# Optimization experiments

Hardware: AMD Instinct MI355X
Metric: run time of the kernel (lower is better)

## Reference

```python
import jax, jax.numpy as jnp
import numpy as np

B, NPIX, M, N_CP, N_CA = 8, 256, 8192, 24576, 24576
EPS = 1e-16


def setup_inputs() -> dict:
    key = jax.random.key(0)
    k1, k2, k3, k4, k5, k6 = jax.random.split(key, 6)
    images = jax.random.normal(k1, (B, NPIX, NPIX), dtype=jnp.float32)
    # k-space trajectory in radians/pixel, range [-pi, pi) as torchkbnufft expects
    ktraj = (jax.random.uniform(k2, (2, M), dtype=jnp.float32) * 2.0 - 1.0) * np.float32(np.pi)
    pulsefac = jax.random.normal(k3, (2, M), dtype=jnp.float32)
    cphase_sign = jnp.sign(jax.random.normal(k4, (3, N_CP), dtype=jnp.float32))
    cphase_ind = jax.random.randint(k5, (3, N_CP), 0, M, dtype=jnp.int32)
    camp_ind = jax.random.randint(k6, (4, N_CA), 0, M, dtype=jnp.int32)
    return {"images": images, "ktraj": ktraj, "pulsefac": pulsefac,
            "cphase_sign": cphase_sign, "cphase_ind": cphase_ind, "camp_ind": camp_ind}


def reference(images, ktraj, pulsefac, cphase_sign, cphase_ind, camp_ind):
    npix = images.shape[-1]
    # centered image coordinates (Fessler NUFFT convention, n_shift = npix//2)
    coords = (jnp.arange(npix) - npix // 2).astype(jnp.float32)
    kv, ku = ktraj[0], ktraj[1]  # (M,) each
    # separable exact NDFT: exp(-i(kv*y + ku*x)) = Ev[m,y] * Eu[m,x]
    Ev = jnp.exp(-1j * kv[:, None] * coords[None, :]).astype(jnp.complex64)  # (M, npix)
    Eu = jnp.exp(-1j * ku[:, None] * coords[None, :]).astype(jnp.complex64)  # (M, npix)
    img_c = images.astype(jnp.complex64)
    tmp = jnp.einsum('byx,my->bmx', img_c, Ev)        # (B, M, npix)
    kdata = jnp.einsum('bmx,mx->bm', tmp, Eu)          # (B, M) complex visibilities
    # pulse-function correction (complex multiply)
    pf = pulsefac[0] + 1j * pulsefac[1]                # (M,)
    vis_c = kdata * pf                                 # (B, M)
    vis = jnp.stack([vis_c.real, vis_c.imag], axis=1)  # (B, 2, M)
    visamp = jnp.sqrt(vis_c.real ** 2 + vis_c.imag ** 2 + EPS)  # (B, M)
    # closure phases: gather triangle visibilities, signed phase sum, degrees
    v_tri = vis_c[:, cphase_ind]                       # (B, 3, N_cp)
    ang = jnp.arctan2(v_tri.imag, v_tri.real)          # (B, 3, N_cp)
    cphase = jnp.einsum('kn,bkn->bn', cphase_sign, ang) * np.float32(180.0 / np.pi)
    # log closure amplitudes: gather quadrangle visibilities
    v_quad = vis_c[:, camp_ind]                        # (B, 4, N_ca)
    amp = jnp.sqrt(v_quad.real ** 2 + v_quad.imag ** 2 + EPS)
    logcamp = (jnp.log(amp[:, 0]) + jnp.log(amp[:, 1])
               - jnp.log(amp[:, 2]) - jnp.log(amp[:, 3]))  # (B, N_ca)
    return vis, visamp, cphase, logcamp
```

## Files before the change

### kernel.cpp

```cpp
#include <hip/hip_runtime.h>
#include <cmath>

#define BB   8
#define NPIX 256
#define MM   8192
#define NCP  24576
#define NCA  24576
#define EPSF 1e-16f

#define KC   32
#define TMB  128
#define NT   512

#define VIS_OFF    0
#define VISAMP_OFF (BB * 2 * MM)
#define CPH_OFF    (VISAMP_OFF + BB * MM)
#define LCA_OFF    (CPH_OFF + BB * NCP)

typedef __bf16 bf16x8 __attribute__((ext_vector_type(8)));
typedef float  f32x4  __attribute__((ext_vector_type(4)));

#define WIDX(row, k8) (((row) >> 4) * 512 + (k8) * 128 + ((row) & 15) * 8)

__device__ __forceinline__ float red2pi(float k, float n)
{
    const double t = (double)k * (double)n * 0.15915494309189535;
    const double f = t - rint(t);
    return (float)(f * 6.283185307179586);
}

__global__ __launch_bounds__(NT, 2)
void nufft_vis_mfma(const float* __restrict__ images,
                    const float* __restrict__ ktraj,
                    const float* __restrict__ pulsefac,
                    float* __restrict__ out)
{
    __shared__ __align__(16) __bf16 sBh[NPIX * KC];
    __shared__ __align__(16) __bf16 sBl[NPIX * KC];

    const int tid  = threadIdx.x;
    const int m0   = blockIdx.x * TMB;
    const int b    = blockIdx.y;
    const int lane = tid & 63;
    const int w    = tid >> 6;
    const int ln15 = lane & 15;
    const int q    = lane >> 4;

    const float kvm = ktraj[m0 + w * 16 + ln15];
    float r1s, r1c, r32s, r32c, as_, ac_;
    sincosf(kvm, &r1s, &r1c);
    sincosf(red2pi(kvm, 32.0f), &r32s, &r32c);
    sincosf(red2pi(kvm, (float)(q * 8 - 128)), &as_, &ac_);
    float anr = ac_, ani = -as_;

    const int bx    = tid & 255;
    const int bhalf = tid >> 8;
    const float* imgb = images + b * NPIX * NPIX + bx;

    f32x4 acc[2][16];
    #pragma unroll
    for (int rt = 0; rt < 2; ++rt)
        #pragma unroll
        for (int ct = 0; ct < 16; ++ct)
            acc[rt][ct] = (f32x4){0.f, 0.f, 0.f, 0.f};

    for (int y0 = 0; y0 < NPIX; y0 += KC) {
        bf16x8 fRh, fRl, fIh, fIl;
        {
            float er = anr, ei = ani;
            #pragma unroll
            for (int j = 0; j < 8; ++j) {
                __bf16 h = (__bf16)er;
                fRh[j] = h; fRl[j] = (__bf16)(er - (float)h);
                h = (__bf16)ei;
                fIh[j] = h; fIl[j] = (__bf16)(ei - (float)h);
                const float nr = er * r1c + ei * r1s;
                const float ni = ei * r1c - er * r1s;
                er = nr; ei = ni;
            }
            const float nr = anr * r32c + ani * r32s;
            const float ni = ani * r32c - anr * r32s;
            anr = nr; ani = ni;
        }
        #pragma unroll
        for (int oo = 0; oo < 2; ++oo) {
            const int oct = bhalf * 2 + oo;
            bf16x8 bh, bl;
            #pragma unroll
            for (int j = 0; j < 8; ++j) {
                const float v = imgb[(y0 + oct * 8 + j) * NPIX];
                const __bf16 h = (__bf16)v;
                bh[j] = h; bl[j] = (__bf16)(v - (float)h);
            }
            const int bo = WIDX(bx, oct);
            *(bf16x8*)&sBh[bo] = bh;
            *(bf16x8*)&sBl[bo] = bl;
        }
        __syncthreads();

        #pragma unroll
        for (int ct = 0; ct < 16; ++ct) {
            const int bro = WIDX(ct * 16 + ln15, q);
            const bf16x8 bh = *(const bf16x8*)&sBh[bro];
            const bf16x8 bl = *(const bf16x8*)&sBl[bro];
            acc[0][ct] = __builtin_amdgcn_mfma_f32_16x16x32_bf16(fRh, bh, acc[0][ct], 0, 0, 0);
            acc[0][ct] = __builtin_amdgcn_mfma_f32_16x16x32_bf16(fRh, bl, acc[0][ct], 0, 0, 0);
            acc[0][ct] = __builtin_amdgcn_mfma_f32_16x16x32_bf16(fRl, bh, acc[0][ct], 0, 0, 0);
            acc[1][ct] = __builtin_amdgcn_mfma_f32_16x16x32_bf16(fIh, bh, acc[1][ct], 0, 0, 0);
            acc[1][ct] = __builtin_amdgcn_mfma_f32_16x16x32_bf16(fIh, bl, acc[1][ct], 0, 0, 0);
            acc[1][ct] = __builtin_amdgcn_mfma_f32_16x16x32_bf16(fIl, bh, acc[1][ct], 0, 0, 0);
        }
        __syncthreads();
    }

    #pragma unroll
    for (int r = 0; r < 4; ++r) {
        const int m = m0 + w * 16 + q * 4 + r;
        const float ku = ktraj[MM + m];
        float s0, c0, s16, c16;
        sincosf(red2pi(ku, (float)(ln15 - 128)), &s0, &c0);
        sincosf(red2pi(ku, 16.0f), &s16, &c16);
        float er = c0, ei = -s0;
        float sr = 0.f, si = 0.f;
        #pragma unroll
        for (int ct = 0; ct < 16; ++ct) {
            const float tr = acc[0][ct][r];
            const float ti = acc[1][ct][r];
            sr = fmaf(tr, er, fmaf(-ti, ei, sr));
            si = fmaf(tr, ei, fmaf(ti, er, si));
            const float nr = er * c16 + ei * s16;
            const float ni = ei * c16 - er * s16;
            er = nr; ei = ni;
        }
        #pragma unroll
        for (int off = 8; off >= 1; off >>= 1) {
            sr += __shfl_xor(sr, off);
            si += __shfl_xor(si, off);
        }
        if (ln15 == 0) {
            const float pr = pulsefac[m];
            const float pi = pulsefac[MM + m];
            const float vr = sr * pr - si * pi;
            const float vi = sr * pi + si * pr;
            out[b * 2 * MM + m]      = vr;
            out[b * 2 * MM + MM + m] = vi;
            out[VISAMP_OFF + b * MM + m] = sqrtf(vr * vr + vi * vi + EPSF);
        }
    }
}

__device__ __forceinline__ float fast_atan2f(float y, float x)
{
    const float ax = fabsf(x), ay = fabsf(y);
    const float mx = fmaxf(ax, ay), mn = fminf(ax, ay);
    const float a  = mn / fmaxf(mx, 1e-37f);
    const float s  = a * a;
    float r = 0.0208351f;
    r = fmaf(r, s, -0.0851330f);
    r = fmaf(r, s,  0.1801410f);
    r = fmaf(r, s, -0.3302995f);
    r = fmaf(r, s,  0.9998660f);
    r *= a;
    r = (ay > ax) ? (1.57079632679f - r) : r;
    r = (x < 0.0f) ? (3.14159265359f - r) : r;
    return (y < 0.0f) ? -r : r;
}

__global__ __launch_bounds__(256)
void gather_fused(const float* __restrict__ vis,
                  const float* __restrict__ sign,
                  const int* __restrict__ cind,
                  const int* __restrict__ caind,
                  float* __restrict__ out)
{
    __shared__ float sv[2 * MM];

    const int i = blockIdx.x * 256 + threadIdx.x;
    const int b = i / NCP;
    const int n = i - b * NCP;

    {
        const float4* g4 = (const float4*)(vis + b * 2 * MM);
        float4* s4 = (float4*)sv;
        #pragma unroll
        for (int j = 0; j < (2 * MM / 4) / 256; ++j)
            s4[j * 256 + threadIdx.x] = g4[j * 256 + threadIdx.x];
    }
    __syncthreads();

    float cp = 0.f;
    #pragma unroll
    for (int k = 0; k < 3; ++k) {
        const int m = cind[k * NCP + n];
        cp += sign[k * NCP + n] * fast_atan2f(sv[MM + m], sv[m]);
    }
    out[CPH_OFF + i] = cp * 57.29577951308232f;

    float p[4];
    #pragma unroll
    for (int k = 0; k < 4; ++k) {
        const int m = caind[k * NCA + n];
        const float vr = sv[m];
        const float vi = sv[MM + m];
        p[k] = vr * vr + vi * vi + EPSF;
    }
    out[LCA_OFF + i] = 0.5f * __logf((p[0] * p[1]) / (p[2] * p[3]));
}

extern "C" void kernel_launch(void* const* d_in, const int* in_sizes, int n_in,
                              void* d_out, int out_size, void* d_ws, size_t ws_size,
                              hipStream_t stream)
{
    const float* images   = (const float*)d_in[0];
    const float* ktraj    = (const float*)d_in[1];
    const float* pulsefac = (const float*)d_in[2];
    const float* csign    = (const float*)d_in[3];
    const int*   cind     = (const int*)d_in[4];
    const int*   caind    = (const int*)d_in[5];
    float* out = (float*)d_out;

    dim3 grid(MM / TMB, BB);
    nufft_vis_mfma<<<grid, NT, 0, stream>>>(images, ktraj, pulsefac, out);
    gather_fused<<<BB * NCP / 256, 256, 0, stream>>>(out, csign, cind, caind, out);
}
```

Before: 116.9 us.

## Software-pipeline image loads and twiddle generation behind MFMA, halve block tile

Halves the block size to 256 threads and 64 k-space rows, so each thread now stages a full image column slice. The next K-chunk's global image loads are issued before the current MFMA loop, and the bf16 split conversion and next A-fragment twiddle generation run after it, all with a fully unrolled chunk loop. The aim is to hide global load latency and VALU work behind the matrix ops. In exchange, every block now reloads the whole image, doubling image traffic and staging work per output, and register pressure rises under launch bounds of one block per CU.

```diff
diff --git a/kernel.cpp b/kernel.cpp
--- a/kernel.cpp
+++ b/kernel.cpp
@@ -9,8 +9,8 @@
 #define EPSF 1e-16f
 
 #define KC   32
-#define TMB  128
-#define NT   512
+#define TMB  64
+#define NT   256
 
 #define VIS_OFF    0
 #define VISAMP_OFF (BB * 2 * MM)
@@ -29,7 +29,7 @@
     return (float)(f * 6.283185307179586);
 }
 
-__global__ __launch_bounds__(NT, 2)
+__global__ __launch_bounds__(NT, 1)
 void nufft_vis_mfma(const float* __restrict__ images,
                     const float* __restrict__ ktraj,
                     const float* __restrict__ pulsefac,
@@ -53,9 +53,53 @@
     sincosf(red2pi(kvm, (float)(q * 8 - 128)), &as_, &ac_);
     float anr = ac_, ani = -as_;
 
-    const int bx    = tid & 255;
-    const int bhalf = tid >> 8;
-    const float* imgb = images + b * NPIX * NPIX + bx;
+    const float* imgb = images + b * NPIX * NPIX + tid;
+
+    bf16x8 fRh[2], fRl[2], fIh[2], fIl[2];
+    float  lv[4][8];
+    bf16x8 sbh[4], sbl[4];
+
+    auto genA = [&](int slot) {
+        float er = anr, ei = ani;
+        #pragma unroll
+        for (int j = 0; j < 8; ++j) {
+            __bf16 h = (__bf16)er;
+            fRh[slot][j] = h; fRl[slot][j] = (__bf16)(er - (float)h);
+            h = (__bf16)ei;
+            fIh[slot][j] = h; fIl[slot][j] = (__bf16)(ei - (float)h);
+            const float nr = er * r1c + ei * r1s;
+            const float ni = ei * r1c - er * r1s;
+            er = nr; ei = ni;
+        }
+        const float nr = anr * r32c + ani * r32s;
+        const float ni = ani * r32c - anr * r32s;
+        anr = nr; ani = ni;
+    };
+    auto loadB = [&](int y0) {
+        #pragma unroll
+        for (int oct = 0; oct < 4; ++oct)
+            #pragma unroll
+            for (int j = 0; j < 8; ++j)
+                lv[oct][j] = imgb[(y0 + oct * 8 + j) * NPIX];
+    };
+    auto convB = [&]() {
+        #pragma unroll
+        for (int oct = 0; oct < 4; ++oct)
+            #pragma unroll
+            for (int j = 0; j < 8; ++j) {
+                const float v = lv[oct][j];
+                const __bf16 h = (__bf16)v;
+                sbh[oct][j] = h; sbl[oct][j] = (__bf16)(v - (float)h);
+            }
+    };
+    auto writeB = [&]() {
+        #pragma unroll
+        for (int oct = 0; oct < 4; ++oct) {
+            const int bo = WIDX(tid, oct);
+            *(bf16x8*)&sBh[bo] = sbh[oct];
+            *(bf16x8*)&sBl[bo] = sbl[oct];
+        }
+    };
 
     f32x4 acc[2][16];
     #pragma unroll
@@ -64,53 +108,36 @@
         for (int ct = 0; ct < 16; ++ct)
             acc[rt][ct] = (f32x4){0.f, 0.f, 0.f, 0.f};
 
-    for (int y0 = 0; y0 < NPIX; y0 += KC) {
-        bf16x8 fRh, fRl, fIh, fIl;
-        {
-            float er = anr, ei = ani;
-            #pragma unroll
-            for (int j = 0; j < 8; ++j) {
-                __bf16 h = (__bf16)er;
-                fRh[j] = h; fRl[j] = (__bf16)(er - (float)h);
-                h = (__bf16)ei;
-                fIh[j] = h; fIl[j] = (__bf16)(ei - (float)h);
-                const float nr = er * r1c + ei * r1s;
-                const float ni = ei * r1c - er * r1s;
-                er = nr; ei = ni;
-            }
-            const float nr = anr * r32c + ani * r32s;
-            const float ni = ani * r32c - anr * r32s;
-            anr = nr; ani = ni;
-        }
-        #pragma unroll
-        for (int oo = 0; oo < 2; ++oo) {
-            const int oct = bhalf * 2 + oo;
-            bf16x8 bh, bl;
-            #pragma unroll
-            for (int j = 0; j < 8; ++j) {
-                const float v = imgb[(y0 + oct * 8 + j) * NPIX];
-                const __bf16 h = (__bf16)v;
-                bh[j] = h; bl[j] = (__bf16)(v - (float)h);
-            }
-            const int bo = WIDX(bx, oct);
-            *(bf16x8*)&sBh[bo] = bh;
-            *(bf16x8*)&sBl[bo] = bl;
-        }
+    genA(0);
+    loadB(0);
+    convB();
+    writeB();
+
+    #pragma unroll
+    for (int c = 0; c < 8; ++c) {
+        const int cur = c & 1;
         __syncthreads();
+        if (c < 7) loadB((c + 1) * KC);
 
         #pragma unroll
         for (int ct = 0; ct < 16; ++ct) {
             const int bro = WIDX(ct * 16 + ln15, q);
             const bf16x8 bh = *(const bf16x8*)&sBh[bro];
             const bf16x8 bl = *(const bf16x8*)&sBl[bro];
-            acc[0][ct] = __builtin_amdgcn_mfma_f32_16x16x32_bf16(fRh, bh, acc[0][ct], 0, 0, 0);
-            acc[0][ct] = __builtin_amdgcn_mfma_f32_16x16x32_bf16(fRh, bl, acc[0][ct], 0, 0, 0);
-            acc[0][ct] = __builtin_amdgcn_mfma_f32_16x16x32_bf16(fRl, bh, acc[0][ct], 0, 0, 0);
-            acc[1][ct] = __builtin_amdgcn_mfma_f32_16x16x32_bf16(fIh, bh, acc[1][ct], 0, 0, 0);
-            acc[1][ct] = __builtin_amdgcn_mfma_f32_16x16x32_bf16(fIh, bl, acc[1][ct], 0, 0, 0);
-            acc[1][ct] = __builtin_amdgcn_mfma_f32_16x16x32_bf16(fIl, bh, acc[1][ct], 0, 0, 0);
+            acc[0][ct] = __builtin_amdgcn_mfma_f32_16x16x32_bf16(fRh[cur], bh, acc[0][ct], 0, 0, 0);
+            acc[0][ct] = __builtin_amdgcn_mfma_f32_16x16x32_bf16(fRh[cur], bl, acc[0][ct], 0, 0, 0);
+            acc[0][ct] = __builtin_amdgcn_mfma_f32_16x16x32_bf16(fRl[cur], bh, acc[0][ct], 0, 0, 0);
+            acc[1][ct] = __builtin_amdgcn_mfma_f32_16x16x32_bf16(fIh[cur], bh, acc[1][ct], 0, 0, 0);
+            acc[1][ct] = __builtin_amdgcn_mfma_f32_16x16x32_bf16(fIh[cur], bl, acc[1][ct], 0, 0, 0);
+            acc[1][ct] = __builtin_amdgcn_mfma_f32_16x16x32_bf16(fIl[cur], bh, acc[1][ct], 0, 0, 0);
+        }
+
+        if (c < 7) {
+            genA(cur ^ 1);
+            convB();
         }
         __syncthreads();
+        if (c < 7) writeB();
     }
 
     #pragma unroll
```

Result: slower. 142.3 us (+21.7%).

## Switch NUFFT GEMM to 32x32x16 MFMA with swapped operands and 2D wave tiling

Applied to the files above, without the earlier changes.

Replaces the 16x16x32 MFMA tiling with 32x32x16 MFMA. The image tile becomes the A operand and the per-lane trajectory phase vector becomes B. Waves are split 4x2 over m and x, and a cross-wave reduction through shared memory is added at the end. The Eu phase-rotation epilogue is rewritten to match the new accumulator layout. The aim is higher MFMA throughput per instruction and less LDS traffic per flop, at the cost of an extra reduction step and a more complex phase recurrence.

```diff
diff --git a/kernel.cpp b/kernel.cpp
--- a/kernel.cpp
+++ b/kernel.cpp
@@ -19,8 +19,9 @@
 
 typedef __bf16 bf16x8 __attribute__((ext_vector_type(8)));
 typedef float  f32x4  __attribute__((ext_vector_type(4)));
-
-#define WIDX(row, k8) (((row) >> 4) * 512 + (k8) * 128 + ((row) & 15) * 8)
+typedef float  f32x16 __attribute__((ext_vector_type(16)));
+
+#define WIDX32(x, o) (((x) >> 5) * 1024 + (o) * 256 + ((x) & 31) * 8)
 
 __device__ __forceinline__ float red2pi(float k, float n)
 {
@@ -43,45 +44,55 @@
     const int b    = blockIdx.y;
     const int lane = tid & 63;
     const int w    = tid >> 6;
-    const int ln15 = lane & 15;
-    const int q    = lane >> 4;
-
-    const float kvm = ktraj[m0 + w * 16 + ln15];
-    float r1s, r1c, r32s, r32c, as_, ac_;
+    const int wm   = w >> 1;
+    const int wx   = w & 1;
+    const int l31  = lane & 31;
+    const int hi   = lane >> 5;
+
+    const int mlane = m0 + wm * 32 + l31;
+    const float kvm = ktraj[mlane];
+    float r1s, r1c, r16s, r16c, as_, ac_;
     sincosf(kvm, &r1s, &r1c);
-    sincosf(red2pi(kvm, 32.0f), &r32s, &r32c);
-    sincosf(red2pi(kvm, (float)(q * 8 - 128)), &as_, &ac_);
+    sincosf(red2pi(kvm, 16.0f), &r16s, &r16c);
+    sincosf(red2pi(kvm, (float)(hi * 8 - 128)), &as_, &ac_);
     float anr = ac_, ani = -as_;
 
     const int bx    = tid & 255;
     const int bhalf = tid >> 8;
     const float* imgb = images + b * NPIX * NPIX + bx;
 
-    f32x4 acc[2][16];
+    auto genB = [&](bf16x8& Rh, bf16x8& Rl, bf16x8& Ih, bf16x8& Il) {
+        float er = anr, ei = ani;
+        #pragma unroll
+        for (int j = 0; j < 8; ++j) {
+            __bf16 h = (__bf16)er;
+            Rh[j] = h; Rl[j] = (__bf16)(er - (float)h);
+            h = (__bf16)ei;
+            Ih[j] = h; Il[j] = (__bf16)(ei - (float)h);
+            const float nr = er * r1c + ei * r1s;
+            const float ni = ei * r1c - er * r1s;
+            er = nr; ei = ni;
+        }
+        const float nr = anr * r16c + ani * r16s;
+        const float ni = ani * r16c - anr * r16s;
+        anr = nr; ani = ni;
+    };
+
+    f32x16 acc[2][4];
     #pragma unroll
-    for (int rt = 0; rt < 2; ++rt)
-        #pragma unroll
-        for (int ct = 0; ct < 16; ++ct)
-            acc[rt][ct] = (f32x4){0.f, 0.f, 0.f, 0.f};
-
-    for (int y0 = 0; y0 < NPIX; y0 += KC) {
-        bf16x8 fRh, fRl, fIh, fIl;
-        {
-            float er = anr, ei = ani;
+    for (int p = 0; p < 2; ++p)
+        #pragma unroll
+        for (int xt = 0; xt < 4; ++xt)
             #pragma unroll
-            for (int j = 0; j < 8; ++j) {
-                __bf16 h = (__bf16)er;
-                fRh[j] = h; fRl[j] = (__bf16)(er - (float)h);
-                h = (__bf16)ei;
-                fIh[j] = h; fIl[j] = (__bf16)(ei - (float)h);
-                const float nr = er * r1c + ei * r1s;
-                const float ni = ei * r1c - er * r1s;
-                er = nr; ei = ni;
-            }
-            const float nr = anr * r32c + ani * r32s;
-            const float ni = ani * r32c - anr * r32s;
-            anr = nr; ani = ni;
-        }
+            for (int rg = 0; rg < 16; ++rg)
+                acc[p][xt][rg] = 0.f;
+
+    for (int c = 0; c < NPIX / KC; ++c) {
+        const int y0 = c * KC;
+
+        bf16x8 eRh, eRl, eIh, eIl;
+        genB(eRh, eRl, eIh, eIl);
+
         #pragma unroll
         for (int oo = 0; oo < 2; ++oo) {
             const int oct = bhalf * 2 + oo;
@@ -92,60 +103,88 @@
                 const __bf16 h = (__bf16)v;
                 bh[j] = h; bl[j] = (__bf16)(v - (float)h);
             }
-            const int bo = WIDX(bx, oct);
+            const int bo = WIDX32(bx, oct);
             *(bf16x8*)&sBh[bo] = bh;
             *(bf16x8*)&sBl[bo] = bl;
         }
         __syncthreads();
 
         #pragma unroll
-        for (int ct = 0; ct < 16; ++ct) {
-            const int bro = WIDX(ct * 16 + ln15, q);
-            const bf16x8 bh = *(const bf16x8*)&sBh[bro];
-            const bf16x8 bl = *(const bf16x8*)&sBl[bro];
-            acc[0][ct] = __builtin_amdgcn_mfma_f32_16x16x32_bf16(fRh, bh, acc[0][ct], 0, 0, 0);
-            acc[0][ct] = __builtin_amdgcn_mfma_f32_16x16x32_bf16(fRh, bl, acc[0][ct], 0, 0, 0);
-            acc[0][ct] = __builtin_amdgcn_mfma_f32_16x16x32_bf16(fRl, bh, acc[0][ct], 0, 0, 0);
-            acc[1][ct] = __builtin_amdgcn_mfma_f32_16x16x32_bf16(fIh, bh, acc[1][ct], 0, 0, 0);
-            acc[1][ct] = __builtin_amdgcn_mfma_f32_16x16x32_bf16(fIh, bl, acc[1][ct], 0, 0, 0);
-            acc[1][ct] = __builtin_amdgcn_mfma_f32_16x16x32_bf16(fIl, bh, acc[1][ct], 0, 0, 0);
+        for (int xt = 0; xt < 4; ++xt) {
+            const int aro = (wx * 4 + xt) * 1024 + hi * 256 + l31 * 8;
+            const bf16x8 ah = *(const bf16x8*)&sBh[aro];
+            const bf16x8 al = *(const bf16x8*)&sBl[aro];
+            acc[0][xt] = __builtin_amdgcn_mfma_f32_32x32x16_bf16(ah, eRh, acc[0][xt], 0, 0, 0);
+            acc[0][xt] = __builtin_amdgcn_mfma_f32_32x32x16_bf16(al, eRh, acc[0][xt], 0, 0, 0);
+            acc[0][xt] = __builtin_amdgcn_mfma_f32_32x32x16_bf16(ah, eRl, acc[0][xt], 0, 0, 0);
+            acc[1][xt] = __builtin_amdgcn_mfma_f32_32x32x16_bf16(ah, eIh, acc[1][xt], 0, 0, 0);
+            acc[1][xt] = __builtin_amdgcn_mfma_f32_32x32x16_bf16(al, eIh, acc[1][xt], 0, 0, 0);
+            acc[1][xt] = __builtin_amdgcn_mfma_f32_32x32x16_bf16(ah, eIl, acc[1][xt], 0, 0, 0);
+        }
+
+        genB(eRh, eRl, eIh, eIl);
+
+        #pragma unroll
+        for (int xt = 0; xt < 4; ++xt) {
+            const int aro = (wx * 4 + xt) * 1024 + (2 + hi) * 256 + l31 * 8;
+            const bf16x8 ah = *(const bf16x8*)&sBh[aro];
+            const bf16x8 al = *(const bf16x8*)&sBl[aro];
+            acc[0][xt] = __builtin_amdgcn_mfma_f32_32x32x16_bf16(ah, eRh, acc[0][xt], 0, 0, 0);
+            acc[0][xt] = __builtin_amdgcn_mfma_f32_32x32x16_bf16(al, eRh, acc[0][xt], 0, 0, 0);
+            acc[0][xt] = __builtin_amdgcn_mfma_f32_32x32x16_bf16(ah, eRl, acc[0][xt], 0, 0, 0);
+            acc[1][xt] = __builtin_amdgcn_mfma_f32_32x32x16_bf16(ah, eIh, acc[1][xt], 0, 0, 0);
+            acc[1][xt] = __builtin_amdgcn_mfma_f32_32x32x16_bf16(al, eIh, acc[1][xt], 0, 0, 0);
+            acc[1][xt] = __builtin_amdgcn_mfma_f32_32x32x16_bf16(ah, eIl, acc[1][xt], 0, 0, 0);
         }
         __syncthreads();
     }
 
-    #pragma unroll
-    for (int r = 0; r < 4; ++r) {
-        const int m = m0 + w * 16 + q * 4 + r;
-        const float ku = ktraj[MM + m];
-        float s0, c0, s16, c16;
-        sincosf(red2pi(ku, (float)(ln15 - 128)), &s0, &c0);
-        sincosf(red2pi(ku, 16.0f), &s16, &c16);
-        float er = c0, ei = -s0;
+    {
+        const float kum = ktraj[MM + mlane];
+        float s1u, c1u, s5u, c5u, s0u, c0u;
+        sincosf(kum, &s1u, &c1u);
+        sincosf(red2pi(kum, 5.0f), &s5u, &c5u);
+        sincosf(red2pi(kum, (float)(wx * 128 + 4 * hi - 128)), &s0u, &c0u);
+        float er = c0u, ei = -s0u;
         float sr = 0.f, si = 0.f;
         #pragma unroll
-        for (int ct = 0; ct < 16; ++ct) {
-            const float tr = acc[0][ct][r];
-            const float ti = acc[1][ct][r];
-            sr = fmaf(tr, er, fmaf(-ti, ei, sr));
-            si = fmaf(tr, ei, fmaf(ti, er, si));
-            const float nr = er * c16 + ei * s16;
-            const float ni = ei * c16 - er * s16;
-            er = nr; ei = ni;
-        }
-        #pragma unroll
-        for (int off = 8; off >= 1; off >>= 1) {
-            sr += __shfl_xor(sr, off);
-            si += __shfl_xor(si, off);
-        }
-        if (ln15 == 0) {
-            const float pr = pulsefac[m];
-            const float pi = pulsefac[MM + m];
-            const float vr = sr * pr - si * pi;
-            const float vi = sr * pi + si * pr;
-            out[b * 2 * MM + m]      = vr;
-            out[b * 2 * MM + MM + m] = vi;
-            out[VISAMP_OFF + b * MM + m] = sqrtf(vr * vr + vi * vi + EPSF);
-        }
+        for (int xt = 0; xt < 4; ++xt) {
+            #pragma unroll
+            for (int rg = 0; rg < 16; ++rg) {
+                const float tr = acc[0][xt][rg];
+                const float ti = acc[1][xt][rg];
+                sr = fmaf(tr, er, fmaf(-ti, ei, sr));
+                si = fmaf(tr, ei, fmaf(ti, er, si));
+                const float cs = ((rg & 3) == 3) ? c5u : c1u;
+                const float sn = ((rg & 3) == 3) ? s5u : s1u;
+                const float nr = er * cs + ei * sn;
+                const float ni = ei * cs - er * sn;
+                er = nr; ei = ni;
+            }
+        }
+        sr += __shfl_xor(sr, 32);
+        si += __shfl_xor(si, 32);
+
+        float2* sPart = (float2*)sBh;
+        if (l31 == lane) {
+            sPart[(wm * 32 + l31) * 2 + wx] = make_float2(sr, si);
+        }
+    }
+    __syncthreads();
+    if (tid < TMB) {
+        const float2* sPart = (const float2*)sBh;
+        const float2 p0 = sPart[tid * 2 + 0];
+        const float2 p1 = sPart[tid * 2 + 1];
+        const float sr = p0.x + p1.x;
+        const float si = p0.y + p1.y;
+        const int m = m0 + tid;
+        const float pr = pulsefac[m];
+        const float pi = pulsefac[MM + m];
+        const float vr = sr * pr - si * pi;
+        const float vi = sr * pi + si * pr;
+        out[b * 2 * MM + m]      = vr;
+        out[b * 2 * MM + MM + m] = vi;
+        out[VISAMP_OFF + b * MM + m] = sqrtf(vr * vr + vi * vi + EPSF);
     }
 }
 
```

After: 120.7 us. +3.2%, slower.
